# Kernel optimization log

Measured on AMD Instinct MI355X. Metric: run time of the kernel, lower is better.

Reference implementation:

```python
import jax, jax.numpy as jnp
import numpy as np

N_BRANCH, N_LAYER = 4, 3
B, T, D_IN = 4, 1024, 32
D_MODEL, D_INNER, D_STATE, D_CONV, DT_RANK = 128, 256, 16, 4, 8
EMBED = 64
MAX_NORM = 10.0  # safe_expmap0 tangent-norm clip
EPS = 1e-7


def setup_inputs() -> dict:
    key = jax.random.key(0)
    ks = jax.random.split(key, 12)
    def nrm(k, shp, s=0.02):
        return s * jax.random.normal(k, shp, dtype=jnp.float32)
    A_init = jnp.log(jnp.arange(1, D_STATE + 1, dtype=jnp.float32))
    return {
        "trend": jax.random.normal(ks[0], (B, T, D_IN), jnp.float32),
        "seasonal_coarse": jax.random.normal(ks[1], (B, T, D_IN), jnp.float32),
        "seasonal_fine": jax.random.normal(ks[2], (B, T, D_IN), jnp.float32),
        "residual": jax.random.normal(ks[3], (B, T, D_IN), jnp.float32),
        "W_ip": nrm(ks[4], (N_BRANCH, D_IN, D_MODEL)),
        "b_ip": jnp.zeros((N_BRANCH, D_MODEL), jnp.float32),
        "W_in": nrm(ks[5], (N_BRANCH, N_LAYER, D_MODEL, 2 * D_INNER)),
        "conv_w": nrm(ks[6], (N_BRANCH, N_LAYER, D_INNER, D_CONV), 0.1),
        "conv_b": jnp.zeros((N_BRANCH, N_LAYER, D_INNER), jnp.float32),
        "W_x": nrm(ks[7], (N_BRANCH, N_LAYER, D_INNER, DT_RANK + 2 * D_STATE)),
        "W_dt": nrm(ks[8], (N_BRANCH, N_LAYER, DT_RANK, D_INNER), 0.1),
        "b_dt": jnp.full((N_BRANCH, N_LAYER, D_INNER), -4.6, jnp.float32),  # softplus ~ 0.01
        "A_log": jnp.broadcast_to(A_init, (N_BRANCH, N_LAYER, D_INNER, D_STATE)),
        "D_param": jnp.ones((N_BRANCH, N_LAYER, D_INNER), jnp.float32),
        "W_out": nrm(ks[9], (N_BRANCH, N_LAYER, D_INNER, D_MODEL)),
        "W_op": nrm(ks[10], (N_BRANCH, D_MODEL, EMBED)),
        "b_op": jnp.zeros((N_BRANCH, EMBED), jnp.float32),
        "eff_scale": jnp.asarray(0.1, jnp.float32),
    }


def _mamba_layer(x, Win, cw, cb, Wx, Wdt, bdt, Alog, Dp, Wout):
    # x: [B, T, d_model]
    Tlen = x.shape[1]
    xz = x @ Win                                   # [B,T,2*di]
    xp, z = jnp.split(xz, 2, axis=-1)
    # causal depthwise conv1d, kernel D_CONV
    xpad = jnp.pad(xp, ((0, 0), (D_CONV - 1, 0), (0, 0)))
    xc = sum(xpad[:, k:k + Tlen, :] * cw[:, k] for k in range(D_CONV))
    xc = jax.nn.silu(xc + cb)                      # [B,T,di]
    dbl = xc @ Wx                                  # [B,T,r+2s]
    dt = jax.nn.softplus(dbl[..., :DT_RANK] @ Wdt + bdt)   # [B,T,di]
    Bm = dbl[..., DT_RANK:DT_RANK + D_STATE]       # [B,T,s]
    Cm = dbl[..., DT_RANK + D_STATE:]              # [B,T,s]
    A = -jnp.exp(Alog)                             # [di,s]
    dA = jnp.exp(dt[..., None] * A)                # [B,T,di,s]
    dBx = (dt * xc)[..., None] * Bm[:, :, None, :] # [B,T,di,s]

    def step(h, inp):
        dA_t, dBx_t, C_t = inp
        h = dA_t * h + dBx_t
        return h, jnp.einsum('bds,bs->bd', h, C_t)

    h0 = jnp.zeros((x.shape[0], D_INNER, D_STATE), x.dtype)
    _, ys = jax.lax.scan(step, h0, (jnp.swapaxes(dA, 0, 1),
                                     jnp.swapaxes(dBx, 0, 1),
                                     jnp.swapaxes(Cm, 0, 1)))
    y = jnp.swapaxes(ys, 0, 1) + Dp * xc
    return (y * jax.nn.silu(z)) @ Wout


def _embed(x, Wip, bip, Wins, cws, cbs, Wxs, Wdts, bdts, Alogs, Dps, Wouts, Wop, bop):
    h = x @ Wip + bip
    for l in range(N_LAYER):
        h = _mamba_layer(h, Wins[l], cws[l], cbs[l], Wxs[l], Wdts[l], bdts[l],
                         Alogs[l], Dps[l], Wouts[l])
    return h.mean(axis=1) @ Wop + bop              # [B, EMBED]


def _expmap0(v):
    # safe expmap0 on Lorentz (k=1): clip tangent norm at MAX_NORM
    n = jnp.linalg.norm(v, axis=-1, keepdims=True)
    nc = jnp.clip(n, EPS, MAX_NORM)
    v = v * (nc / jnp.maximum(n, EPS))
    return jnp.concatenate([jnp.cosh(nc), jnp.sinh(nc) / nc * v], axis=-1)


def _projx(x):
    sp = x[..., 1:]
    t = jnp.sqrt(1.0 + jnp.sum(sp * sp, axis=-1, keepdims=True))
    return jnp.concatenate([t, sp], axis=-1)


def _logmap0(x):
    sp = x[..., 1:]
    t = jnp.maximum(x[..., :1], 1.0 + EPS)
    d = jnp.arccosh(t)
    spn = jnp.maximum(jnp.linalg.norm(sp, axis=-1, keepdims=True), EPS)
    return d * sp / spn


def _forward(trend, seasonal_coarse, seasonal_fine, residual,
             W_ip, b_ip, W_in, conv_w, conv_b, W_x, W_dt, b_dt,
             A_log, D_param, W_out, W_op, b_op, eff_scale):
    xs = [trend, seasonal_coarse, seasonal_fine, residual]
    z_t = [
        _embed(xs[b], W_ip[b], b_ip[b], W_in[b], conv_w[b], conv_b[b], W_x[b],
               W_dt[b], b_dt[b], A_log[b], D_param[b], W_out[b], W_op[b], b_op[b])
        for b in range(N_BRANCH)
    ]
    es = jnp.tanh(eff_scale)
    z_h = [_projx(_expmap0(z * es)) for z in z_t]
    us = [_logmap0(zh) for zh in z_h]
    combined_tangent = us[0] + us[1] + us[2] + us[3]
    combined_h = _projx(_expmap0(combined_tangent * es))
    return (*z_t, *z_h, combined_tangent, combined_h)


def reference(trend, seasonal_coarse, seasonal_fine, residual,
              W_ip, b_ip, W_in, conv_w, conv_b, W_x, W_dt, b_dt,
              A_log, D_param, W_out, W_op, b_op, eff_scale):
    return _forward(trend, seasonal_coarse, seasonal_fine, residual,
                    W_ip, b_ip, W_in, conv_w, conv_b, W_x, W_dt, b_dt,
                    A_log, D_param, W_out, W_op, b_op, eff_scale)
```

## Files before the change

### kernel.cpp

```cpp
#include <hip/hip_runtime.h>
#include <math.h>

#define NBR 4
#define NLAY 3
#define Bk 4
#define Tk 1024
#define DIN 32
#define DMODEL 128
#define DINNER 256
#define DSTATE 16
#define DTRANK 8
#define EMBEDk 64
#define BT (Bk*Tk)
#define EPSF 1e-7f
#define MAXNF 10.0f
#define LCH 32
#define NCH (Tk/LCH)
#define UF 8
#define NWB 320

typedef __bf16 bf16x8 __attribute__((ext_vector_type(8)));
typedef float  f32x4  __attribute__((ext_vector_type(4)));
typedef unsigned short u16x8 __attribute__((ext_vector_type(8)));
typedef unsigned short u16x4 __attribute__((ext_vector_type(4)));

__device__ __forceinline__ float siluf(float x){ return x / (1.f + __expf(-x)); }
__device__ __forceinline__ float softplusf(float x){ return (x > 20.f) ? x : log1pf(__expf(x)); }
__device__ __forceinline__ unsigned short f2b(float x){
    union { float f; unsigned u; } v; v.f = x;
    unsigned r = v.u + 0x7FFF + ((v.u >> 16) & 1);
    return (unsigned short)(r >> 16);
}
__device__ __forceinline__ float b2f(unsigned short u){
    union { unsigned u; float f; } v; v.u = ((unsigned)u) << 16; return v.f;
}

__device__ __forceinline__ void dA_pow(float q, float* dA){
    dA[0] = q;             dA[1] = q * q;
    dA[2] = dA[1] * dA[0]; dA[3] = dA[1] * dA[1];
    dA[4] = dA[3] * dA[0]; dA[5] = dA[3] * dA[1];
    dA[6] = dA[3] * dA[2]; dA[7] = dA[3] * dA[3];
    #pragma unroll
    for (int s = 8; s < 16; ++s) dA[s] = dA[s - 8] * dA[7];
}
__device__ __forceinline__ void dA_exp(float dtv, const float* Aa, float* dA){
    #pragma unroll
    for (int s = 0; s < 16; ++s) dA[s] = __expf(dtv * Aa[s]);
}

template<int MODE>
__global__ __launch_bounds__(256) void bgemm_k(
    const unsigned short* __restrict__ Ab, long aBr, int K,
    const unsigned short* __restrict__ Bt, long bBr,
    float* __restrict__ C1, long c1Br,
    unsigned short* __restrict__ Cb, long cbBr,
    unsigned short* __restrict__ Cb2, long cb2Br,
    float* __restrict__ Mb,
    const float* __restrict__ bias, long biasBr)
{
    const int br = blockIdx.z;
    Ab += (long)br * aBr;
    Bt += (long)br * bBr;
    if (MODE == 0) { Cb += (long)br * cbBr; Cb2 += (long)br * cb2Br; }
    if (MODE == 3) { Cb += (long)br * cbBr; C1 += (long)br * c1Br;
                     bias += (long)br * biasBr; }
    if (MODE == 1) { Mb += (long)br * (Bk * DMODEL); }
    const int m0 = blockIdx.x * 64, n0 = blockIdx.y * 64;
    __shared__ __align__(16) unsigned short As[16 * 64 * 8];
    __shared__ __align__(16) unsigned short Bs[16 * 64 * 8];
    const int tid = threadIdx.x;
    const int lane = tid & 63, w = tid >> 6;
    const int wm = w >> 1, wn = w & 1;
    const int quad = lane >> 4, l15 = lane & 15;
    f32x4 acc00 = {0,0,0,0}, acc01 = {0,0,0,0}, acc10 = {0,0,0,0}, acc11 = {0,0,0,0};
    for (int kc = 0; kc < K; kc += 128) {
        #pragma unroll
        for (int it = 0; it < 4; ++it) {
            const int c = tid + it * 256;
            const int r = c & 63, kch = c >> 6;
            *(u16x8*)&As[(kch * 64 + r) * 8] =
                *(const u16x8*)(Ab + (long)(m0 + r) * K + kc + kch * 8);
            *(u16x8*)&Bs[(kch * 64 + r) * 8] =
                *(const u16x8*)(Bt + (long)(n0 + r) * K + kc + kch * 8);
        }
        __syncthreads();
        #pragma unroll
        for (int k0 = 0; k0 < 128; k0 += 32) {
            const int kch = (k0 >> 3) + quad;
            bf16x8 a0 = *(const bf16x8*)&As[(kch * 64 + wm * 32 +      l15) * 8];
            bf16x8 a1 = *(const bf16x8*)&As[(kch * 64 + wm * 32 + 16 + l15) * 8];
            bf16x8 b0 = *(const bf16x8*)&Bs[(kch * 64 + wn * 32 +      l15) * 8];
            bf16x8 b1 = *(const bf16x8*)&Bs[(kch * 64 + wn * 32 + 16 + l15) * 8];
            acc00 = __builtin_amdgcn_mfma_f32_16x16x32_bf16(a0, b0, acc00, 0, 0, 0);
            acc01 = __builtin_amdgcn_mfma_f32_16x16x32_bf16(a0, b1, acc01, 0, 0, 0);
            acc10 = __builtin_amdgcn_mfma_f32_16x16x32_bf16(a1, b0, acc10, 0, 0, 0);
            acc11 = __builtin_amdgcn_mfma_f32_16x16x32_bf16(a1, b1, acc11, 0, 0, 0);
        }
        __syncthreads();
    }
    if (MODE == 1) {
        float s0 = 0.f, s1 = 0.f;
        #pragma unroll
        for (int r = 0; r < 4; ++r) { s0 += acc00[r] + acc10[r];
                                      s1 += acc01[r] + acc11[r]; }
        const int bidx = m0 >> 10;
        atomicAdd(&Mb[bidx * DMODEL + n0 + wn * 32 + l15], s0);
        atomicAdd(&Mb[bidx * DMODEL + n0 + wn * 32 + 16 + l15], s1);
        return;
    }
    #pragma unroll
    for (int e = 0; e < 4; ++e) {
        f32x4 a = (e == 0) ? acc00 : (e == 1) ? acc01 : (e == 2) ? acc10 : acc11;
        const int msub = (e >> 1) * 16, nsub = (e & 1) * 16;
        const int col = n0 + wn * 32 + nsub + l15;
        #pragma unroll
        for (int r = 0; r < 4; ++r) {
            const int row = m0 + wm * 32 + msub + quad * 4 + r;
            const float v = a[r];
            if (MODE == 0) {
                if (n0 < 256) Cb[(long)row * 256 + col] = f2b(v);
                else          Cb2[(long)row * 256 + (col - 256)] = f2b(siluf(v));
            } else {
                if (col < 256)      Cb[(long)row * 256 + col] = f2b(softplusf(v + bias[col]));
                else if (col < 288) C1[(long)row * 32 + (col - 256)] = v;
            }
        }
    }
}

__device__ void transposeTile(const float* __restrict__ W,
                              unsigned short* __restrict__ o,
                              int Kd, int Nd, int n0, int k0, float* smem)
{
    float (*tile)[65] = (float(*)[65])smem;
    const int t = threadIdx.x;
    #pragma unroll
    for (int i = 0; i < 16; ++i) {
        int idx = t + i * 256;
        int kl = idx >> 6, nl = idx & 63;
        tile[kl][nl] = W[(long)(k0 + kl) * Nd + n0 + nl];
    }
    __syncthreads();
    #pragma unroll
    for (int i = 0; i < 16; ++i) {
        int idx = t + i * 256;
        int nl = idx >> 6, kl = idx & 63;
        o[(long)(n0 + nl) * Kd + k0 + kl] = f2b(tile[kl][nl]);
    }
}

__global__ __launch_bounds__(256) void prep_k(
    const float* __restrict__ W_in, const float* __restrict__ W_out,
    const float* __restrict__ W_x, const float* __restrict__ W_dt,
    const float* __restrict__ X0, const float* __restrict__ X1,
    const float* __restrict__ X2, const float* __restrict__ X3,
    const float* __restrict__ W_ip, const float* __restrict__ b_ip,
    unsigned short* __restrict__ Win0T, unsigned short* __restrict__ Wo2T,
    unsigned short* __restrict__ WcT, unsigned short* __restrict__ h_bf,
    unsigned short* __restrict__ WfT, unsigned* __restrict__ zbuf)
{
    __shared__ float smem[32 * 68 * 2];
    const int id = blockIdx.x;
    if (id < 64) {
        int br = id >> 4, rem = id & 15;
        int nt = rem & 7, kt = rem >> 3;
        transposeTile(W_in + (long)br * NLAY * DMODEL * 512,
                      Win0T + (long)br * 512 * DMODEL,
                      DMODEL, 512, nt * 64, kt * 64, smem);
    } else if (id < 96) {
        int id3 = id - 64;
        int br = id3 >> 3, rem = id3 & 7;
        int nt = rem & 1, kt = rem >> 1;
        transposeTile(W_out + ((long)br * NLAY + 2) * DINNER * DMODEL,
                      Wo2T + (long)br * DMODEL * DINNER,
                      DINNER, DMODEL, nt * 64, kt * 64, smem);
    } else if (id < 3936) {
        int id4 = id - 96;
        int bl = id4 / NWB, n = id4 % NWB;
        const int k = threadIdx.x;
        const float* WxP = W_x + (long)bl * DINNER * 40;
        float v;
        if (n < 256) {
            const float* WdtP = W_dt + (long)bl * DTRANK * DINNER;
            float s = 0.f;
            #pragma unroll
            for (int r = 0; r < 8; ++r)
                s = fmaf(WxP[k * 40 + r], WdtP[r * DINNER + n], s);
            v = s;
        } else if (n < 288) {
            v = WxP[k * 40 + 8 + (n - 256)];
        } else {
            v = 0.f;
        }
        WcT[(long)bl * NWB * DINNER + (long)n * DINNER + k] = f2b(v);
    } else if (id < 4448) {
        int id5 = id - 3936;
        int br = id5 >> 7, rem = id5 & 127;
        int m0 = (rem & 63) * 64, n0 = (rem >> 6) * 64;
        const float* A = (br == 1) ? X1 : (br == 2) ? X2 : (br == 3) ? X3 : X0;
        const float* Bw = W_ip + (long)br * DIN * DMODEL;
        const float* bias = b_ip + (long)br * DMODEL;
        unsigned short* Cb = h_bf + (long)br * BT * DMODEL;
        float (*As)[68] = (float(*)[68])smem;
        float (*Bs)[68] = (float(*)[68])(smem + 32 * 68);
        const int tid = threadIdx.x;
        const int tx = tid & 15, ty = tid >> 4;
        float acc[4][4] = {};
        #pragma unroll
        for (int it = 0; it < 2; ++it) {
            int idd = tid + it * 256;
            int r = idd >> 3, c4 = (idd & 7) << 2;
            float4 v = *(const float4*)(A + (long)(m0 + r) * DIN + c4);
            As[c4+0][r] = v.x; As[c4+1][r] = v.y; As[c4+2][r] = v.z; As[c4+3][r] = v.w;
            int rb = idd >> 4, cb = (idd & 15) << 2;
            *(float4*)&Bs[rb][cb] = *(const float4*)(Bw + (long)rb * DMODEL + n0 + cb);
        }
        __syncthreads();
        #pragma unroll
        for (int kk = 0; kk < 32; ++kk) {
            float4 a4 = *(const float4*)&As[kk][ty << 2];
            float4 b4 = *(const float4*)&Bs[kk][tx << 2];
            float av[4] = {a4.x, a4.y, a4.z, a4.w};
            float bv[4] = {b4.x, b4.y, b4.z, b4.w};
            #pragma unroll
            for (int i = 0; i < 4; ++i)
                #pragma unroll
                for (int j = 0; j < 4; ++j)
                    acc[i][j] = fmaf(av[i], bv[j], acc[i][j]);
        }
        const int col = n0 + (tx << 2);
        #pragma unroll
        for (int i = 0; i < 4; ++i) {
            const int row = m0 + (ty << 2) + i;
            #pragma unroll
            for (int j = 0; j < 4; ++j)
                Cb[(long)row * DMODEL + col + j] = f2b(acc[i][j] + bias[col + j]);
        }
    } else {
        if (id == 4448) {
            for (int i = threadIdx.x; i < 4096; i += 256) zbuf[i] = 0u;
        }
        int sid = id - 4448;
        int z = sid >> 5, rem = sid & 31;
        int mt = rem >> 3, nt = rem & 7;
        const int p = z >> 2, br = z & 3;
        const float* A  = W_out + (long)(br * NLAY + p) * DINNER * DMODEL;
        const float* Bw = W_in  + (long)(br * NLAY + p + 1) * DMODEL * 512;
        unsigned short* WfTz = WfT + (long)z * 512 * DINNER;
        const int m0 = mt * 64, n0 = nt * 64;
        float (*As)[68] = (float(*)[68])smem;
        float (*Bs)[68] = (float(*)[68])(smem + 32 * 68);
        const int tid = threadIdx.x;
        const int tx = tid & 15, ty = tid >> 4;
        float acc[4][4] = {};
        for (int kc = 0; kc < DMODEL; kc += 32) {
            #pragma unroll
            for (int it = 0; it < 2; ++it) {
                int idd = tid + it * 256;
                int r = idd >> 3, c4 = (idd & 7) << 2;
                float4 v = *(const float4*)(A + (long)(m0 + r) * DMODEL + kc + c4);
                As[c4+0][r] = v.x; As[c4+1][r] = v.y; As[c4+2][r] = v.z; As[c4+3][r] = v.w;
                int rb = idd >> 4, cb = (idd & 15) << 2;
                *(float4*)&Bs[rb][cb] = *(const float4*)(Bw + (long)(kc + rb) * 512 + n0 + cb);
            }
            __syncthreads();
            #pragma unroll
            for (int kk = 0; kk < 32; ++kk) {
                float4 a4 = *(const float4*)&As[kk][ty << 2];
                float4 b4 = *(const float4*)&Bs[kk][tx << 2];
                float av[4] = {a4.x, a4.y, a4.z, a4.w};
                float bv[4] = {b4.x, b4.y, b4.z, b4.w};
                #pragma unroll
                for (int i = 0; i < 4; ++i)
                    #pragma unroll
                    for (int j = 0; j < 4; ++j)
                        acc[i][j] = fmaf(av[i], bv[j], acc[i][j]);
            }
            __syncthreads();
        }
        const int row0 = m0 + (ty << 2);
        const int col0 = n0 + (tx << 2);
        #pragma unroll
        for (int j = 0; j < 4; ++j) {
            u16x4 t4;
            #pragma unroll
            for (int i = 0; i < 4; ++i) t4[i] = f2b(acc[i][j]);
            *(u16x4*)&WfTz[(long)(col0 + j) * DINNER + row0] = t4;
        }
    }
}

__global__ __launch_bounds__(256) void conv_k(
    const unsigned short* __restrict__ xp, const float* __restrict__ cw,
    const float* __restrict__ cb, unsigned short* __restrict__ xcb, int layer)
{
    const int br = blockIdx.y;
    const long base = (long)br * BT * DINNER;
    const int idx = blockIdx.x * 256 + threadIdx.x;
    const int d = idx & (DINNER - 1);
    const int row = idx >> 8;
    const int t = row & (Tk - 1);
    const float4 w4 = *(const float4*)(cw + ((long)(br * NLAY + layer) * DINNER + d) * 4);
    const float wv[4] = {w4.x, w4.y, w4.z, w4.w};
    float acc = cb[(br * NLAY + layer) * DINNER + d];
    const unsigned short* xpb = xp + base + idx;
    #pragma unroll
    for (int k = 0; k < 4; ++k) {
        int tt = t + k - 3;
        if (tt >= 0) acc = fmaf(b2f(xpb[(long)(k - 3) * DINNER]), wv[k], acc);
    }
    xcb[base + idx] = f2b(siluf(acc));
}

__global__ __launch_bounds__(256) void scan1_k(
    const unsigned short* __restrict__ dtb, const unsigned short* __restrict__ xcb,
    const float* __restrict__ bcb, const float* __restrict__ Alog,
    float* __restrict__ recbuf, int layer)
{
    const int c = blockIdx.x, b = blockIdx.y, br = blockIdx.z;
    const int d = threadIdx.x;
    const float* Ap = Alog + ((long)(br * NLAY + layer) * DINNER + d) * DSTATE;
    float Aa[16];
    bool pw = true;
    #pragma unroll
    for (int s = 0; s < 16; ++s) {
        Aa[s] = -__expf(Ap[s]);
        pw = pw && (fabsf(Aa[s] + (float)(s + 1)) < 1e-3f);
    }
    const long rbase = (long)br * BT + (long)b * Tk + (long)c * LCH;
    const unsigned short* dtp = dtb + rbase * DINNER + d;
    const unsigned short* xcp = xcb + rbase * DINNER + d;
    __shared__ float bcs[LCH * 32];
    {
        const float4* g = (const float4*)(bcb + rbase * 32);
        ((float4*)bcs)[d] = g[d];
    }
    float dtc[UF], xcc[UF];
    #pragma unroll
    for (int u = 0; u < UF; ++u) {
        dtc[u] = b2f(dtp[(long)u * DINNER]);
        xcc[u] = b2f(xcp[(long)u * DINNER]);
    }
    __syncthreads();
    float h[16];
    #pragma unroll
    for (int s = 0; s < 16; ++s) h[s] = 0.f;
    float sumdt = 0.f;
    for (int base = 0; base < LCH; base += UF) {
        const int nb = (base + UF < LCH) ? base + UF : base;
        float dtn[UF], xcn[UF];
        #pragma unroll
        for (int u = 0; u < UF; ++u) {
            dtn[u] = b2f(dtp[(long)(nb + u) * DINNER]);
            xcn[u] = b2f(xcp[(long)(nb + u) * DINNER]);
        }
        #pragma unroll
        for (int u = 0; u < UF; ++u) {
            const int t = base + u;
            const float dtv = dtc[u];
            const float dtxc = dtv * xcc[u];
            sumdt += dtv;
            float dA[16];
            if (pw) dA_pow(__expf(-dtv), dA);
            else    dA_exp(dtv, Aa, dA);
            const float* bcT = bcs + t * 32;
            #pragma unroll
            for (int s = 0; s < 16; ++s)
                h[s] = fmaf(dA[s], h[s], dtxc * bcT[s]);
        }
        #pragma unroll
        for (int u = 0; u < UF; ++u) { dtc[u] = dtn[u]; xcc[u] = xcn[u]; }
    }
    float* sb = recbuf + (((long)(br * 4 + b) * (NCH - 1) + c) * 17) * 256 + d;
    #pragma unroll
    for (int s = 0; s < 16; ++s) sb[s * 256] = h[s];
    sb[16 * 256] = sumdt;
}

__global__ __launch_bounds__(256) void scan3_k(
    const unsigned short* __restrict__ dtb, const unsigned short* __restrict__ xcb,
    const float* __restrict__ bcb, const unsigned short* __restrict__ zb,
    const float* __restrict__ Alog, const float* __restrict__ Dpar,
    const float* __restrict__ recbuf, unsigned short* __restrict__ yzb, int layer)
{
    const int c = blockIdx.x, b = blockIdx.y, br = blockIdx.z;
    const int d = threadIdx.x;
    const float* Ap = Alog + ((long)(br * NLAY + layer) * DINNER + d) * DSTATE;
    float Aa[16];
    bool pw = true;
    #pragma unroll
    for (int s = 0; s < 16; ++s) {
        Aa[s] = -__expf(Ap[s]);
        pw = pw && (fabsf(Aa[s] + (float)(s + 1)) < 1e-3f);
    }
    float h[16];
    #pragma unroll
    for (int s = 0; s < 16; ++s) h[s] = 0.f;
    if (c > 0) {
        const float* recB = recbuf + ((long)(br * 4 + b) * (NCH - 1)) * 17 * 256 + d;
        float rh[16], rs;
        #pragma unroll
        for (int s = 0; s < 16; ++s) rh[s] = recB[s * 256];
        rs = recB[16 * 256];
        for (int cc = 0; cc < c; ++cc) {
            float nh[16], ns = 0.f;
            if (cc + 1 < c) {
                const float* r2 = recB + (long)(cc + 1) * 17 * 256;
                #pragma unroll
                for (int s = 0; s < 16; ++s) nh[s] = r2[s * 256];
                ns = r2[16 * 256];
            } else {
                #pragma unroll
                for (int s = 0; s < 16; ++s) nh[s] = 0.f;
            }
            float P[16];
            if (pw) dA_pow(__expf(-rs), P);
            else    dA_exp(rs, Aa, P);
            #pragma unroll
            for (int s = 0; s < 16; ++s) h[s] = fmaf(h[s], P[s], rh[s]);
            #pragma unroll
            for (int s = 0; s < 16; ++s) rh[s] = nh[s];
            rs = ns;
        }
    }
    const float Dp = Dpar[(br * NLAY + layer) * DINNER + d];
    const long rbase = (long)br * BT + (long)b * Tk + (long)c * LCH;
    const unsigned short* dtp = dtb + rbase * DINNER + d;
    const unsigned short* xcp = xcb + rbase * DINNER + d;
    const unsigned short* zp  = zb  + rbase * DINNER + d;
    unsigned short* yp = yzb + rbase * DINNER + d;
    __shared__ float bcs[LCH * 32];
    {
        const float4* g = (const float4*)(bcb + rbase * 32);
        ((float4*)bcs)[d] = g[d];
    }
    float dtc[UF], xcc[UF], zc[UF];
    #pragma unroll
    for (int u = 0; u < UF; ++u) {
        dtc[u] = b2f(dtp[(long)u * DINNER]);
        xcc[u] = b2f(xcp[(long)u * DINNER]);
        zc[u]  = b2f(zp[(long)u * DINNER]);
    }
    __syncthreads();
    for (int base = 0; base < LCH; base += UF) {
        const int nb = (base + UF < LCH) ? base + UF : base;
        float dtn[UF], xcn[UF], zn[UF];
        #pragma unroll
        for (int u = 0; u < UF; ++u) {
            dtn[u] = b2f(dtp[(long)(nb + u) * DINNER]);
            xcn[u] = b2f(xcp[(long)(nb + u) * DINNER]);
            zn[u]  = b2f(zp[(long)(nb + u) * DINNER]);
        }
        #pragma unroll
        for (int u = 0; u < UF; ++u) {
            const int t = base + u;
            const float dtv = dtc[u], xcv = xcc[u];
            const float dtxc = dtv * xcv;
            float dA[16];
            if (pw) dA_pow(__expf(-dtv), dA);
            else    dA_exp(dtv, Aa, dA);
            const float* bcT = bcs + t * 32;
            #pragma unroll
            for (int s = 0; s < 16; ++s)
                h[s] = fmaf(dA[s], h[s], dtxc * bcT[s]);
            float y0 = 0.f, y1 = 0.f, y2 = 0.f, y3 = 0.f;
            #pragma unroll
            for (int s = 0; s < 16; s += 4) {
                y0 = fmaf(h[s+0], bcT[16+s+0], y0);
                y1 = fmaf(h[s+1], bcT[16+s+1], y1);
                y2 = fmaf(h[s+2], bcT[16+s+2], y2);
                y3 = fmaf(h[s+3], bcT[16+s+3], y3);
            }
            const float y = (y0 + y1) + (y2 + y3) + Dp * xcv;
            yp[(long)t * DINNER] = f2b(y * zc[u]);
        }
        #pragma unroll
        for (int u = 0; u < UF; ++u) { dtc[u] = dtn[u]; xcc[u] = xcn[u]; zc[u] = zn[u]; }
    }
}

__global__ __launch_bounds__(64) void final_k(
    const float* __restrict__ Mb, const float* __restrict__ Wop,
    const float* __restrict__ bop, float* __restrict__ out,
    const float* __restrict__ eff)
{
    __shared__ float hm[NBR * Bk * DMODEL];
    __shared__ float zts[NBR * Bk * EMBEDk];
    __shared__ float us[NBR][Bk][EMBEDk];
    const int t = threadIdx.x;
    for (int i = t; i < NBR * Bk * DMODEL; i += 64) hm[i] = Mb[i] * (1.0f / Tk);
    __syncthreads();
    for (int br = 0; br < NBR; ++br) {
        const float* wp = Wop + (long)br * DMODEL * EMBEDk + t;
        const float bb = bop[br * EMBEDk + t];
        for (int b = 0; b < Bk; ++b) {
            const float* hmp = &hm[(br * Bk + b) * DMODEL];
            float acc = bb;
            for (int k = 0; k < DMODEL; ++k) acc = fmaf(hmp[k], wp[k * EMBEDk], acc);
            out[(br * Bk + b) * EMBEDk + t] = acc;
            zts[(br * Bk + b) * EMBEDk + t] = acc;
        }
    }
    __syncthreads();
    const float es = tanhf(eff[0]);
    if (t < 16) {
        const int br = t >> 2, b = t & 3;
        const float* z = &zts[(br * Bk + b) * EMBEDk];
        float n2 = 0.f;
        for (int e = 0; e < EMBEDk; ++e) { float v = z[e] * es; n2 = fmaf(v, v, n2); }
        const float n  = sqrtf(n2);
        const float nc = fminf(fmaxf(n, EPSF), MAXNF);
        const float sc = nc / fmaxf(n, EPSF);
        const float sh = sinhf(nc) / nc;
        const float fac = es * sc * sh;
        float* zh = out + 1024 + br * (Bk * (EMBEDk + 1)) + b * (EMBEDk + 1);
        float sp2 = 0.f;
        for (int e = 0; e < EMBEDk; ++e) {
            float spv = z[e] * fac;
            sp2 = fmaf(spv, spv, sp2);
            zh[1 + e] = spv;
            us[br][b][e] = spv;
        }
        const float t0 = sqrtf(1.f + sp2);
        zh[0] = t0;
        const float dd  = acoshf(fmaxf(t0, 1.f + EPSF));
        const float spn = fmaxf(sqrtf(sp2), EPSF);
        const float rr  = dd / spn;
        for (int e = 0; e < EMBEDk; ++e) us[br][b][e] *= rr;
    }
    __syncthreads();
    if (t < 4) {
        const int b = t;
        float ct[EMBEDk];
        float* cto = out + 2064 + b * EMBEDk;
        for (int e = 0; e < EMBEDk; ++e) {
            float v = us[0][b][e] + us[1][b][e] + us[2][b][e] + us[3][b][e];
            ct[e] = v; cto[e] = v;
        }
        float n2 = 0.f;
        for (int e = 0; e < EMBEDk; ++e) { float v = ct[e] * es; n2 = fmaf(v, v, n2); }
        const float n  = sqrtf(n2);
        const float nc = fminf(fmaxf(n, EPSF), MAXNF);
        const float sc = nc / fmaxf(n, EPSF);
        const float sh = sinhf(nc) / nc;
        const float fac = es * sc * sh;
        float* ch = out + 2320 + b * (EMBEDk + 1);
        float sp2 = 0.f;
        for (int e = 0; e < EMBEDk; ++e) {
            float spv = ct[e] * fac;
            sp2 = fmaf(spv, spv, sp2);
            ch[1 + e] = spv;
        }
        ch[0] = sqrtf(1.f + sp2);
    }
}

extern "C" void kernel_launch(void* const* d_in, const int* in_sizes, int n_in,
                              void* d_out, int out_size, void* d_ws, size_t ws_size,
                              hipStream_t stream)
{
    const float* X0 = (const float*)d_in[0];
    const float* X1 = (const float*)d_in[1];
    const float* X2 = (const float*)d_in[2];
    const float* X3 = (const float*)d_in[3];
    const float* W_ip   = (const float*)d_in[4];
    const float* b_ip   = (const float*)d_in[5];
    const float* W_in   = (const float*)d_in[6];
    const float* conv_w = (const float*)d_in[7];
    const float* conv_b = (const float*)d_in[8];
    const float* W_x    = (const float*)d_in[9];
    const float* W_dt   = (const float*)d_in[10];
    const float* b_dt   = (const float*)d_in[11];
    const float* A_log  = (const float*)d_in[12];
    const float* D_par  = (const float*)d_in[13];
    const float* W_out  = (const float*)d_in[14];
    const float* W_op   = (const float*)d_in[15];
    const float* b_op   = (const float*)d_in[16];
    const float* eff    = (const float*)d_in[17];
    float* out = (float*)d_out;
    float* ws  = (float*)d_ws;

    float* meanb  = ws + 1024;
    float* buf_bc = ws + 4096;
    float* recbuf = buf_bc + (long)NBR * BT * 32;
    unsigned short* dt_bf = (unsigned short*)(recbuf + (long)16 * (NCH - 1) * 17 * 256);
    unsigned short* h_bf  = dt_bf + (long)NBR * BT * DINNER;
    unsigned short* xp_bf = h_bf  + (long)NBR * BT * DMODEL;
    unsigned short* z_bf  = xp_bf + (long)NBR * BT * DINNER;
    unsigned short* xc_bf = z_bf  + (long)NBR * BT * DINNER;
    unsigned short* yz_bf = xc_bf + (long)NBR * BT * DINNER;
    unsigned short* Win0T = yz_bf + (long)NBR * BT * DINNER;
    unsigned short* WfT   = Win0T + (long)NBR * 512 * DMODEL;
    unsigned short* Wo2T  = WfT   + (long)8 * 512 * DINNER;
    unsigned short* WcT   = Wo2T  + (long)NBR * DMODEL * DINNER;

    prep_k<<<4704, 256, 0, stream>>>(
        W_in, W_out, W_x, W_dt, X0, X1, X2, X3, W_ip, b_ip,
        Win0T, Wo2T, WcT, h_bf, WfT, (unsigned*)ws);

    for (int l = 0; l < NLAY; ++l) {
        if (l == 0) {
            bgemm_k<0><<<dim3(BT / 64, 8, NBR), 256, 0, stream>>>(
                h_bf, (long)BT * DMODEL, DMODEL, Win0T, (long)512 * DMODEL,
                nullptr, 0,
                xp_bf, (long)BT * DINNER, z_bf, (long)BT * DINNER,
                nullptr, nullptr, 0);
        } else {
            bgemm_k<0><<<dim3(BT / 64, 8, NBR), 256, 0, stream>>>(
                yz_bf, (long)BT * DINNER, DINNER,
                WfT + (long)(l - 1) * 4 * 512 * DINNER, (long)512 * DINNER,
                nullptr, 0,
                xp_bf, (long)BT * DINNER, z_bf, (long)BT * DINNER,
                nullptr, nullptr, 0);
        }
        conv_k<<<dim3((BT * DINNER) / 256, NBR), 256, 0, stream>>>(
            xp_bf, conv_w, conv_b, xc_bf, l);
        bgemm_k<3><<<dim3(BT / 64, NWB / 64, NBR), 256, 0, stream>>>(
            xc_bf, (long)BT * DINNER, DINNER,
            WcT + (long)l * NWB * DINNER, (long)NLAY * NWB * DINNER,
            buf_bc, (long)BT * 32,
            dt_bf, (long)BT * DINNER, nullptr, 0,
            nullptr, b_dt + l * DINNER, (long)NLAY * DINNER);
        scan1_k<<<dim3(NCH - 1, Bk, NBR), 256, 0, stream>>>(
            dt_bf, xc_bf, buf_bc, A_log, recbuf, l);
        scan3_k<<<dim3(NCH, Bk, NBR), 256, 0, stream>>>(
            dt_bf, xc_bf, buf_bc, z_bf, A_log, D_par, recbuf, yz_bf, l);
        if (l == NLAY - 1) {
            bgemm_k<1><<<dim3(BT / 64, DMODEL / 64, NBR), 256, 0, stream>>>(
                yz_bf, (long)BT * DINNER, DINNER,
                Wo2T, (long)DMODEL * DINNER,
                nullptr, 0, nullptr, 0, nullptr, 0,
                meanb, nullptr, 0);
        }
    }

    final_k<<<1, 64, 0, stream>>>(meanb, W_op, b_op, out, eff);
}
```

Baseline: 482.0 us.

## Fuse causal conv into dt/BC GEMM and scans; fold final out-projection into mean

Removes the standalone conv kernel and xc buffer: the depthwise causal conv plus SiLU is recomputed on the fly inside the dt/BC GEMM's A-tile load and inside both scan kernels from xp. The last layer's out-projection GEMM is replaced by accumulating the time-sum of yz per channel in the scan via atomics, then applying W_out to the mean in the final kernel, using linearity. This cuts memory traffic and two launches, at the cost of redundant conv arithmetic, larger register arrays in the scans, and a heavier single-block final kernel.

```diff
diff --git a/kernel.cpp b/kernel.cpp
--- a/kernel.cpp
+++ b/kernel.cpp
@@ -16,7 +16,6 @@
 #define MAXNF 10.0f
 #define LCH 32
 #define NCH (Tk/LCH)
-#define UF 8
 #define NWB 320
 
 typedef __bf16 bf16x8 __attribute__((ext_vector_type(8)));
@@ -48,23 +47,16 @@
     for (int s = 0; s < 16; ++s) dA[s] = __expf(dtv * Aa[s]);
 }
 
-template<int MODE>
-__global__ __launch_bounds__(256) void bgemm_k(
+__global__ __launch_bounds__(256) void xz_k(
     const unsigned short* __restrict__ Ab, long aBr, int K,
     const unsigned short* __restrict__ Bt, long bBr,
-    float* __restrict__ C1, long c1Br,
-    unsigned short* __restrict__ Cb, long cbBr,
-    unsigned short* __restrict__ Cb2, long cb2Br,
-    float* __restrict__ Mb,
-    const float* __restrict__ bias, long biasBr)
+    unsigned short* __restrict__ Cxp, unsigned short* __restrict__ Cz)
 {
     const int br = blockIdx.z;
     Ab += (long)br * aBr;
     Bt += (long)br * bBr;
-    if (MODE == 0) { Cb += (long)br * cbBr; Cb2 += (long)br * cb2Br; }
-    if (MODE == 3) { Cb += (long)br * cbBr; C1 += (long)br * c1Br;
-                     bias += (long)br * biasBr; }
-    if (MODE == 1) { Mb += (long)br * (Bk * DMODEL); }
+    Cxp += (long)br * BT * DINNER;
+    Cz  += (long)br * BT * DINNER;
     const int m0 = blockIdx.x * 64, n0 = blockIdx.y * 64;
     __shared__ __align__(16) unsigned short As[16 * 64 * 8];
     __shared__ __align__(16) unsigned short Bs[16 * 64 * 8];
@@ -98,16 +90,6 @@
         }
         __syncthreads();
     }
-    if (MODE == 1) {
-        float s0 = 0.f, s1 = 0.f;
-        #pragma unroll
-        for (int r = 0; r < 4; ++r) { s0 += acc00[r] + acc10[r];
-                                      s1 += acc01[r] + acc11[r]; }
-        const int bidx = m0 >> 10;
-        atomicAdd(&Mb[bidx * DMODEL + n0 + wn * 32 + l15], s0);
-        atomicAdd(&Mb[bidx * DMODEL + n0 + wn * 32 + 16 + l15], s1);
-        return;
-    }
     #pragma unroll
     for (int e = 0; e < 4; ++e) {
         f32x4 a = (e == 0) ? acc00 : (e == 1) ? acc01 : (e == 2) ? acc10 : acc11;
@@ -117,13 +99,97 @@
         for (int r = 0; r < 4; ++r) {
             const int row = m0 + wm * 32 + msub + quad * 4 + r;
             const float v = a[r];
-            if (MODE == 0) {
-                if (n0 < 256) Cb[(long)row * 256 + col] = f2b(v);
-                else          Cb2[(long)row * 256 + (col - 256)] = f2b(siluf(v));
-            } else {
-                if (col < 256)      Cb[(long)row * 256 + col] = f2b(softplusf(v + bias[col]));
-                else if (col < 288) C1[(long)row * 32 + (col - 256)] = v;
+            if (n0 < 256) Cxp[(long)row * 256 + col] = f2b(v);
+            else          Cz[(long)row * 256 + (col - 256)] = f2b(siluf(v));
+        }
+    }
+}
+
+__global__ __launch_bounds__(256) void dtbc_k(
+    const unsigned short* __restrict__ xp, const unsigned short* __restrict__ WcT,
+    const float* __restrict__ conv_w, const float* __restrict__ conv_b,
+    const float* __restrict__ b_dt,
+    unsigned short* __restrict__ dtb, float* __restrict__ bcb, int layer)
+{
+    const int br = blockIdx.z;
+    const int bl = br * NLAY + layer;
+    xp  += (long)br * BT * DINNER;
+    WcT += (long)bl * NWB * DINNER;
+    dtb += (long)br * BT * DINNER;
+    bcb += (long)br * BT * 32;
+    const float* bias = b_dt + (long)bl * DINNER;
+    const int m0 = blockIdx.x * 64, n0 = blockIdx.y * 64;
+    __shared__ __align__(16) unsigned short As[16 * 64 * 8];
+    __shared__ __align__(16) unsigned short Bs[16 * 64 * 8];
+    __shared__ float cw_s[256][4];
+    __shared__ float cb_s[256];
+    const int tid = threadIdx.x;
+    {
+        const float4 w = *(const float4*)(conv_w + ((long)bl * DINNER + tid) * 4);
+        cw_s[tid][0] = w.x; cw_s[tid][1] = w.y; cw_s[tid][2] = w.z; cw_s[tid][3] = w.w;
+        cb_s[tid] = conv_b[bl * DINNER + tid];
+    }
+    __syncthreads();
+    const int lane = tid & 63, w = tid >> 6;
+    const int wm = w >> 1, wn = w & 1;
+    const int quad = lane >> 4, l15 = lane & 15;
+    f32x4 acc00 = {0,0,0,0}, acc01 = {0,0,0,0}, acc10 = {0,0,0,0}, acc11 = {0,0,0,0};
+    for (int kc = 0; kc < DINNER; kc += 128) {
+        #pragma unroll
+        for (int it = 0; it < 4; ++it) {
+            const int c = tid + it * 256;
+            const int r = c & 63, kch = c >> 6;
+            const int row = m0 + r;
+            const int tb = row & (Tk - 1);
+            const int d0 = kc + kch * 8;
+            u16x8 xr[4];
+            #pragma unroll
+            for (int k = 0; k < 4; ++k) {
+                if (tb + k - 3 >= 0)
+                    xr[k] = *(const u16x8*)(xp + (long)(row + k - 3) * DINNER + d0);
+                else
+                    xr[k] = (u16x8){0,0,0,0,0,0,0,0};
             }
+            u16x8 o;
+            #pragma unroll
+            for (int j = 0; j < 8; ++j) {
+                const int d = d0 + j;
+                float a = cb_s[d];
+                #pragma unroll
+                for (int k = 0; k < 4; ++k)
+                    a = fmaf(b2f(xr[k][j]), cw_s[d][k], a);
+                o[j] = f2b(siluf(a));
+            }
+            *(u16x8*)&As[(kch * 64 + r) * 8] = o;
+            *(u16x8*)&Bs[(kch * 64 + r) * 8] =
+                *(const u16x8*)(WcT + (long)(n0 + r) * DINNER + kc + kch * 8);
+        }
+        __syncthreads();
+        #pragma unroll
+        for (int k0 = 0; k0 < 128; k0 += 32) {
+            const int kch = (k0 >> 3) + quad;
+            bf16x8 a0 = *(const bf16x8*)&As[(kch * 64 + wm * 32 +      l15) * 8];
+            bf16x8 a1 = *(const bf16x8*)&As[(kch * 64 + wm * 32 + 16 + l15) * 8];
+            bf16x8 b0 = *(const bf16x8*)&Bs[(kch * 64 + wn * 32 +      l15) * 8];
+            bf16x8 b1 = *(const bf16x8*)&Bs[(kch * 64 + wn * 32 + 16 + l15) * 8];
+            acc00 = __builtin_amdgcn_mfma_f32_16x16x32_bf16(a0, b0, acc00, 0, 0, 0);
+            acc01 = __builtin_amdgcn_mfma_f32_16x16x32_bf16(a0, b1, acc01, 0, 0, 0);
+            acc10 = __builtin_amdgcn_mfma_f32_16x16x32_bf16(a1, b0, acc10, 0, 0, 0);
+            acc11 = __builtin_amdgcn_mfma_f32_16x16x32_bf16(a1, b1, acc11, 0, 0, 0);
+        }
+        __syncthreads();
+    }
+    #pragma unroll
+    for (int e = 0; e < 4; ++e) {
+        f32x4 a = (e == 0) ? acc00 : (e == 1) ? acc01 : (e == 2) ? acc10 : acc11;
+        const int msub = (e >> 1) * 16, nsub = (e & 1) * 16;
+        const int col = n0 + wn * 32 + nsub + l15;
+        #pragma unroll
+        for (int r = 0; r < 4; ++r) {
+            const int row = m0 + wm * 32 + msub + quad * 4 + r;
+            const float v = a[r];
+            if (col < 256)      dtb[(long)row * 256 + col] = f2b(softplusf(v + bias[col]));
+            else if (col < 288) bcb[(long)row * 32 + (col - 256)] = v;
         }
     }
 }
@@ -155,9 +221,9 @@
     const float* __restrict__ X0, const float* __restrict__ X1,
     const float* __restrict__ X2, const float* __restrict__ X3,
     const float* __restrict__ W_ip, const float* __restrict__ b_ip,
-    unsigned short* __restrict__ Win0T, unsigned short* __restrict__ Wo2T,
-    unsigned short* __restrict__ WcT, unsigned short* __restrict__ h_bf,
-    unsigned short* __restrict__ WfT, unsigned* __restrict__ zbuf)
+    unsigned short* __restrict__ Win0T, unsigned short* __restrict__ WcT,
+    unsigned short* __restrict__ h_bf, unsigned short* __restrict__ WfT,
+    unsigned* __restrict__ zbuf)
 {
     __shared__ float smem[32 * 68 * 2];
     const int id = blockIdx.x;
@@ -167,15 +233,8 @@
         transposeTile(W_in + (long)br * NLAY * DMODEL * 512,
                       Win0T + (long)br * 512 * DMODEL,
                       DMODEL, 512, nt * 64, kt * 64, smem);
-    } else if (id < 96) {
-        int id3 = id - 64;
-        int br = id3 >> 3, rem = id3 & 7;
-        int nt = rem & 1, kt = rem >> 1;
-        transposeTile(W_out + ((long)br * NLAY + 2) * DINNER * DMODEL,
-                      Wo2T + (long)br * DMODEL * DINNER,
-                      DINNER, DMODEL, nt * 64, kt * 64, smem);
-    } else if (id < 3936) {
-        int id4 = id - 96;
+    } else if (id < 3904) {
+        int id4 = id - 64;
         int bl = id4 / NWB, n = id4 % NWB;
         const int k = threadIdx.x;
         const float* WxP = W_x + (long)bl * DINNER * 40;
@@ -193,8 +252,8 @@
             v = 0.f;
         }
         WcT[(long)bl * NWB * DINNER + (long)n * DINNER + k] = f2b(v);
-    } else if (id < 4448) {
-        int id5 = id - 3936;
+    } else if (id < 4416) {
+        int id5 = id - 3904;
         int br = id5 >> 7, rem = id5 & 127;
         int m0 = (rem & 63) * 64, n0 = (rem >> 6) * 64;
         const float* A = (br == 1) ? X1 : (br == 2) ? X2 : (br == 3) ? X3 : X0;
@@ -237,10 +296,10 @@
                 Cb[(long)row * DMODEL + col + j] = f2b(acc[i][j] + bias[col + j]);
         }
     } else {
-        if (id == 4448) {
+        if (id == 4416) {
             for (int i = threadIdx.x; i < 4096; i += 256) zbuf[i] = 0u;
         }
-        int sid = id - 4448;
+        int sid = id - 4416;
         int z = sid >> 5, rem = sid & 31;
         int mt = rem >> 3, nt = rem & 7;
         const int p = z >> 2, br = z & 3;
@@ -290,36 +349,16 @@
     }
 }
 
-__global__ __launch_bounds__(256) void conv_k(
-    const unsigned short* __restrict__ xp, const float* __restrict__ cw,
-    const float* __restrict__ cb, unsigned short* __restrict__ xcb, int layer)
-{
-    const int br = blockIdx.y;
-    const long base = (long)br * BT * DINNER;
-    const int idx = blockIdx.x * 256 + threadIdx.x;
-    const int d = idx & (DINNER - 1);
-    const int row = idx >> 8;
-    const int t = row & (Tk - 1);
-    const float4 w4 = *(const float4*)(cw + ((long)(br * NLAY + layer) * DINNER + d) * 4);
-    const float wv[4] = {w4.x, w4.y, w4.z, w4.w};
-    float acc = cb[(br * NLAY + layer) * DINNER + d];
-    const unsigned short* xpb = xp + base + idx;
-    #pragma unroll
-    for (int k = 0; k < 4; ++k) {
-        int tt = t + k - 3;
-        if (tt >= 0) acc = fmaf(b2f(xpb[(long)(k - 3) * DINNER]), wv[k], acc);
-    }
-    xcb[base + idx] = f2b(siluf(acc));
-}
-
 __global__ __launch_bounds__(256) void scan1_k(
-    const unsigned short* __restrict__ dtb, const unsigned short* __restrict__ xcb,
-    const float* __restrict__ bcb, const float* __restrict__ Alog,
+    const unsigned short* __restrict__ dtb, const unsigned short* __restrict__ xpb,
+    const float* __restrict__ bcb, const float* __restrict__ cw,
+    const float* __restrict__ cbp, const float* __restrict__ Alog,
     float* __restrict__ recbuf, int layer)
 {
     const int c = blockIdx.x, b = blockIdx.y, br = blockIdx.z;
     const int d = threadIdx.x;
-    const float* Ap = Alog + ((long)(br * NLAY + layer) * DINNER + d) * DSTATE;
+    const int bl = br * NLAY + layer;
+    const float* Ap = Alog + ((long)bl * DINNER + d) * DSTATE;
     float Aa[16];
     bool pw = true;
     #pragma unroll
@@ -328,48 +367,48 @@
         pw = pw && (fabsf(Aa[s] + (float)(s + 1)) < 1e-3f);
     }
     const long rbase = (long)br * BT + (long)b * Tk + (long)c * LCH;
+    __shared__ float bcs[LCH * 32];
+    ((float4*)bcs)[d] = ((const float4*)(bcb + rbase * 32))[d];
+    const unsigned short* xpp = xpb + rbase * DINNER + d;
     const unsigned short* dtp = dtb + rbase * DINNER + d;
-    const unsigned short* xcp = xcb + rbase * DINNER + d;
-    __shared__ float bcs[LCH * 32];
-    {
-        const float4* g = (const float4*)(bcb + rbase * 32);
-        ((float4*)bcs)[d] = g[d];
-    }
-    float dtc[UF], xcc[UF];
-    #pragma unroll
-    for (int u = 0; u < UF; ++u) {
-        dtc[u] = b2f(dtp[(long)u * DINNER]);
-        xcc[u] = b2f(xcp[(long)u * DINNER]);
+    const float4 w4 = *(const float4*)(cw + ((long)bl * DINNER + d) * 4);
+    const float cbv = cbp[bl * DINNER + d];
+    float xpv[LCH + 3];
+    #pragma unroll
+    for (int i = 0; i < LCH + 3; ++i) {
+        const int tl = i - 3;
+        xpv[i] = (c * LCH + tl >= 0) ? b2f(xpp[(long)tl * DINNER]) : 0.f;
+    }
+    float dtv[LCH];
+    #pragma unroll
+    for (int t = 0; t < LCH; ++t) dtv[t] = b2f(dtp[(long)t * DINNER]);
+    float xcv[LCH];
+    #pragma unroll
+    for (int t = 0; t < LCH; ++t) {
+        float a = cbv;
+        a = fmaf(xpv[t],     w4.x, a);
+        a = fmaf(xpv[t + 1], w4.y, a);
+        a = fmaf(xpv[t + 2], w4.z, a);
+        a = fmaf(xpv[t + 3], w4.w, a);
+        xcv[t] = siluf(a);
     }
     __syncthreads();
     float h[16];
     #pragma unroll
     for (int s = 0; s < 16; ++s) h[s] = 0.f;
     float sumdt = 0.f;
-    for (int base = 0; base < LCH; base += UF) {
-        const int nb = (base + UF < LCH) ? base + UF : base;
-        float dtn[UF], xcn[UF];
-        #pragma unroll
-        for (int u = 0; u < UF; ++u) {
-            dtn[u] = b2f(dtp[(long)(nb + u) * DINNER]);
-            xcn[u] = b2f(xcp[(long)(nb + u) * DINNER]);
-        }
-        #pragma unroll
-        for (int u = 0; u < UF; ++u) {
-            const int t = base + u;
-            const float dtv = dtc[u];
-            const float dtxc = dtv * xcc[u];
-            sumdt += dtv;
-            float dA[16];
-            if (pw) dA_pow(__expf(-dtv), dA);
-            else    dA_exp(dtv, Aa, dA);
-            const float* bcT = bcs + t * 32;
-            #pragma unroll
-            for (int s = 0; s < 16; ++s)
-                h[s] = fmaf(dA[s], h[s], dtxc * bcT[s]);
-        }
-        #pragma unroll
-        for (int u = 0; u < UF; ++u) { dtc[u] = dtn[u]; xcc[u] = xcn[u]; }
+    #pragma unroll
+    for (int t = 0; t < LCH; ++t) {
+        const float dtval = dtv[t];
+        const float dtxc = dtval * xcv[t];
+        sumdt += dtval;
+        float dA[16];
+        if (pw) dA_pow(__expf(-dtval), dA);
+        else    dA_exp(dtval, Aa, dA);
+        const float* bcT = bcs + t * 32;
+        #pragma unroll
+        for (int s = 0; s < 16; ++s)
+            h[s] = fmaf(dA[s], h[s], dtxc * bcT[s]);
     }
     float* sb = recbuf + (((long)(br * 4 + b) * (NCH - 1) + c) * 17) * 256 + d;
     #pragma unroll
@@ -378,14 +417,17 @@
 }
 
 __global__ __launch_bounds__(256) void scan3_k(
-    const unsigned short* __restrict__ dtb, const unsigned short* __restrict__ xcb,
+    const unsigned short* __restrict__ dtb, const unsigned short* __restrict__ xpb,
     const float* __restrict__ bcb, const unsigned short* __restrict__ zb,
+    const float* __restrict__ cw, const float* __restrict__ cbp,
     const float* __restrict__ Alog, const float* __restrict__ Dpar,
-    const float* __restrict__ recbuf, unsigned short* __restrict__ yzb, int layer)
+    const float* __restrict__ recbuf, unsigned short* __restrict__ yzb,
+    float* __restrict__ Macc, int layer)
 {
     const int c = blockIdx.x, b = blockIdx.y, br = blockIdx.z;
     const int d = threadIdx.x;
-    const float* Ap = Alog + ((long)(br * NLAY + layer) * DINNER + d) * DSTATE;
+    const int bl = br * NLAY + layer;
+    const float* Ap = Alog + ((long)bl * DINNER + d) * DSTATE;
     float Aa[16];
     bool pw = true;
     #pragma unroll
@@ -393,6 +435,38 @@
         Aa[s] = -__expf(Ap[s]);
         pw = pw && (fabsf(Aa[s] + (float)(s + 1)) < 1e-3f);
     }
+    const long rbase = (long)br * BT + (long)b * Tk + (long)c * LCH;
+    __shared__ float bcs[LCH * 32];
+    ((float4*)bcs)[d] = ((const float4*)(bcb + rbase * 32))[d];
+    const unsigned short* xpp = xpb + rbase * DINNER + d;
+    const unsigned short* dtp = dtb + rbase * DINNER + d;
+    const unsigned short* zp  = zb  + rbase * DINNER + d;
+    unsigned short* yp = yzb + rbase * DINNER + d;
+    const float4 w4 = *(const float4*)(cw + ((long)bl * DINNER + d) * 4);
+    const float cbv = cbp[bl * DINNER + d];
+    float xpv[LCH + 3];
+    #pragma unroll
+    for (int i = 0; i < LCH + 3; ++i) {
+        const int tl = i - 3;
+        xpv[i] = (c * LCH + tl >= 0) ? b2f(xpp[(long)tl * DINNER]) : 0.f;
+    }
+    float dtv[LCH], zv[LCH];
+    #pragma unroll
+    for (int t = 0; t < LCH; ++t) {
+        dtv[t] = b2f(dtp[(long)t * DINNER]);
+        zv[t]  = b2f(zp[(long)t * DINNER]);
+    }
+    float xcv[LCH];
+    #pragma unroll
+    for (int t = 0; t < LCH; ++t) {
+        float a = cbv;
+        a = fmaf(xpv[t],     w4.x, a);
+        a = fmaf(xpv[t + 1], w4.y, a);
+        a = fmaf(xpv[t + 2], w4.z, a);
+        a = fmaf(xpv[t + 3], w4.w, a);
+        xcv[t] = siluf(a);
+    }
+    __syncthreads();
     float h[16];
     #pragma unroll
     for (int s = 0; s < 16; ++s) h[s] = 0.f;
@@ -423,83 +497,66 @@
             rs = ns;
         }
     }
-    const float Dp = Dpar[(br * NLAY + layer) * DINNER + d];
-    const long rbase = (long)br * BT + (long)b * Tk + (long)c * LCH;
-    const unsigned short* dtp = dtb + rbase * DINNER + d;
-    const unsigned short* xcp = xcb + rbase * DINNER + d;
-    const unsigned short* zp  = zb  + rbase * DINNER + d;
-    unsigned short* yp = yzb + rbase * DINNER + d;
-    __shared__ float bcs[LCH * 32];
-    {
-        const float4* g = (const float4*)(bcb + rbase * 32);
-        ((float4*)bcs)[d] = g[d];
-    }
-    float dtc[UF], xcc[UF], zc[UF];
-    #pragma unroll
-    for (int u = 0; u < UF; ++u) {
-        dtc[u] = b2f(dtp[(long)u * DINNER]);
-        xcc[u] = b2f(xcp[(long)u * DINNER]);
-        zc[u]  = b2f(zp[(long)u * DINNER]);
-    }
-    __syncthreads();
-    for (int base = 0; base < LCH; base += UF) {
-        const int nb = (base + UF < LCH) ? base + UF : base;
-        float dtn[UF], xcn[UF], zn[UF];
-        #pragma unroll
-        for (int u = 0; u < UF; ++u) {
-            dtn[u] = b2f(dtp[(long)(nb + u) * DINNER]);
-            xcn[u] = b2f(xcp[(long)(nb + u) * DINNER]);
-            zn[u]  = b2f(zp[(long)(nb + u) * DINNER]);
-        }
-        #pragma unroll
-        for (int u = 0; u < UF; ++u) {
-            const int t = base + u;
-            const float dtv = dtc[u], xcv = xcc[u];
-            const float dtxc = dtv * xcv;
-            float dA[16];
-            if (pw) dA_pow(__expf(-dtv), dA);
-            else    dA_exp(dtv, Aa, dA);
-            const float* bcT = bcs + t * 32;
-            #pragma unroll
-            for (int s = 0; s < 16; ++s)
-                h[s] = fmaf(dA[s], h[s], dtxc * bcT[s]);
-            float y0 = 0.f, y1 = 0.f, y2 = 0.f, y3 = 0.f;
-            #pragma unroll
-            for (int s = 0; s < 16; s += 4) {
-                y0 = fmaf(h[s+0], bcT[16+s+0], y0);
-                y1 = fmaf(h[s+1], bcT[16+s+1], y1);
-                y2 = fmaf(h[s+2], bcT[16+s+2], y2);
-                y3 = fmaf(h[s+3], bcT[16+s+3], y3);
-            }
-            const float y = (y0 + y1) + (y2 + y3) + Dp * xcv;
-            yp[(long)t * DINNER] = f2b(y * zc[u]);
-        }
-        #pragma unroll
-        for (int u = 0; u < UF; ++u) { dtc[u] = dtn[u]; xcc[u] = xcn[u]; zc[u] = zn[u]; }
-    }
-}
-
-__global__ __launch_bounds__(64) void final_k(
-    const float* __restrict__ Mb, const float* __restrict__ Wop,
-    const float* __restrict__ bop, float* __restrict__ out,
-    const float* __restrict__ eff)
-{
-    __shared__ float hm[NBR * Bk * DMODEL];
-    __shared__ float zts[NBR * Bk * EMBEDk];
+    const float Dp = Dpar[bl * DINNER + d];
+    float yzsum = 0.f;
+    #pragma unroll
+    for (int t = 0; t < LCH; ++t) {
+        const float dtval = dtv[t], xcval = xcv[t];
+        const float dtxc = dtval * xcval;
+        float dA[16];
+        if (pw) dA_pow(__expf(-dtval), dA);
+        else    dA_exp(dtval, Aa, dA);
+        const float* bcT = bcs + t * 32;
+        #pragma unroll
+        for (int s = 0; s < 16; ++s)
+            h[s] = fmaf(dA[s], h[s], dtxc * bcT[s]);
+        float y0 = 0.f, y1 = 0.f, y2 = 0.f, y3 = 0.f;
+        #pragma unroll
+        for (int s = 0; s < 16; s += 4) {
+            y0 = fmaf(h[s+0], bcT[16+s+0], y0);
+            y1 = fmaf(h[s+1], bcT[16+s+1], y1);
+            y2 = fmaf(h[s+2], bcT[16+s+2], y2);
+            y3 = fmaf(h[s+3], bcT[16+s+3], y3);
+        }
+        const float y = (y0 + y1) + (y2 + y3) + Dp * xcval;
+        const float yz = y * zv[t];
+        yzsum += yz;
+        yp[(long)t * DINNER] = f2b(yz);
+    }
+    if (Macc) atomicAdd(&Macc[(br * 4 + b) * DINNER + d], yzsum);
+}
+
+__global__ __launch_bounds__(256) void final_k(
+    const float* __restrict__ Macc, const float* __restrict__ W_out,
+    const float* __restrict__ Wop, const float* __restrict__ bop,
+    float* __restrict__ out, const float* __restrict__ eff)
+{
+    __shared__ float ms[16 * 256];
+    __shared__ float mh[16 * 128];
+    __shared__ float zts[16 * 64];
     __shared__ float us[NBR][Bk][EMBEDk];
     const int t = threadIdx.x;
-    for (int i = t; i < NBR * Bk * DMODEL; i += 64) hm[i] = Mb[i] * (1.0f / Tk);
-    __syncthreads();
-    for (int br = 0; br < NBR; ++br) {
-        const float* wp = Wop + (long)br * DMODEL * EMBEDk + t;
-        const float bb = bop[br * EMBEDk + t];
-        for (int b = 0; b < Bk; ++b) {
-            const float* hmp = &hm[(br * Bk + b) * DMODEL];
-            float acc = bb;
-            for (int k = 0; k < DMODEL; ++k) acc = fmaf(hmp[k], wp[k * EMBEDk], acc);
-            out[(br * Bk + b) * EMBEDk + t] = acc;
-            zts[(br * Bk + b) * EMBEDk + t] = acc;
-        }
+    for (int i = t; i < 16 * 256; i += 256) ms[i] = Macc[i] * (1.0f / Tk);
+    __syncthreads();
+    for (int o = t; o < 16 * 128; o += 256) {
+        const int seq = o >> 7, dm = o & 127;
+        const int br = seq >> 2;
+        const float* W2 = W_out + (long)(br * NLAY + 2) * DINNER * DMODEL;
+        float a = 0.f;
+        for (int dd = 0; dd < DINNER; ++dd)
+            a = fmaf(ms[seq * 256 + dd], W2[dd * DMODEL + dm], a);
+        mh[o] = a;
+    }
+    __syncthreads();
+    for (int o = t; o < 16 * 64; o += 256) {
+        const int seq = o >> 6, e = o & 63;
+        const int br = seq >> 2;
+        float a = bop[br * EMBEDk + e];
+        const float* wp = Wop + (long)br * DMODEL * EMBEDk;
+        for (int k = 0; k < DMODEL; ++k)
+            a = fmaf(mh[seq * 128 + k], wp[k * EMBEDk + e], a);
+        out[o] = a;
+        zts[o] = a;
     }
     __syncthreads();
     const float es = tanhf(eff[0]);
@@ -580,59 +637,41 @@
     float* out = (float*)d_out;
     float* ws  = (float*)d_ws;
 
-    float* meanb  = ws + 1024;
+    float* Macc   = ws;
     float* buf_bc = ws + 4096;
     float* recbuf = buf_bc + (long)NBR * BT * 32;
     unsigned short* dt_bf = (unsigned short*)(recbuf + (long)16 * (NCH - 1) * 17 * 256);
     unsigned short* h_bf  = dt_bf + (long)NBR * BT * DINNER;
     unsigned short* xp_bf = h_bf  + (long)NBR * BT * DMODEL;
     unsigned short* z_bf  = xp_bf + (long)NBR * BT * DINNER;
-    unsigned short* xc_bf = z_bf  + (long)NBR * BT * DINNER;
-    unsigned short* yz_bf = xc_bf + (long)NBR * BT * DINNER;
+    unsigned short* yz_bf = z_bf  + (long)NBR * BT * DINNER;
     unsigned short* Win0T = yz_bf + (long)NBR * BT * DINNER;
     unsigned short* WfT   = Win0T + (long)NBR * 512 * DMODEL;
-    unsigned short* Wo2T  = WfT   + (long)8 * 512 * DINNER;
-    unsigned short* WcT   = Wo2T  + (long)NBR * DMODEL * DINNER;
-
-    prep_k<<<4704, 256, 0, stream>>>(
+    unsigned short* WcT   = WfT   + (long)8 * 512 * DINNER;
+
+    prep_k<<<4672, 256, 0, stream>>>(
         W_in, W_out, W_x, W_dt, X0, X1, X2, X3, W_ip, b_ip,
-        Win0T, Wo2T, WcT, h_bf, WfT, (unsigned*)ws);
+        Win0T, WcT, h_bf, WfT, (unsigned*)ws);
 
     for (int l = 0; l < NLAY; ++l) {
         if (l == 0) {
-            bgemm_k<0><<<dim3(BT / 64, 8, NBR), 256, 0, stream>>>(
-                h_bf, (long)BT * DMODEL, DMODEL, Win0T, (long)512 * DMODEL,
-                nullptr, 0,
-                xp_bf, (long)BT * DINNER, z_bf, (long)BT * DINNER,
-                nullptr, nullptr, 0);
+            xz_k<<<dim3(BT / 64, 8, NBR), 256, 0, stream>>>(
+                h_bf, (long)BT * DMODEL, DMODEL,
+                Win0T, (long)512 * DMODEL, xp_bf, z_bf);
         } else {
-            bgemm_k<0><<<dim3(BT / 64, 8, NBR), 256, 0, stream>>>(
+            xz_k<<<dim3(BT / 64, 8, NBR), 256, 0, stream>>>(
                 yz_bf, (long)BT * DINNER, DINNER,
                 WfT + (long)(l - 1) * 4 * 512 * DINNER, (long)512 * DINNER,
-                nullptr, 0,
-                xp_bf, (long)BT * DINNER, z_bf, (long)BT * DINNER,
-                nullptr, nullptr, 0);
-        }
-        conv_k<<<dim3((BT * DINNER) / 256, NBR), 256, 0, stream>>>(
-            xp_bf, conv_w, conv_b, xc_bf, l);
-        bgemm_k<3><<<dim3(BT / 64, NWB / 64, NBR), 256, 0, stream>>>(
-            xc_bf, (long)BT * DINNER, DINNER,
-            WcT + (long)l * NWB * DINNER, (long)NLAY * NWB * DINNER,
-            buf_bc, (long)BT * 32,
-            dt_bf, (long)BT * DINNER, nullptr, 0,
-            nullptr, b_dt + l * DINNER, (long)NLAY * DINNER);
+                xp_bf, z_bf);
+        }
+        dtbc_k<<<dim3(BT / 64, NWB / 64, NBR), 256, 0, stream>>>(
+            xp_bf, WcT, conv_w, conv_b, b_dt, dt_bf, buf_bc, l);
         scan1_k<<<dim3(NCH - 1, Bk, NBR), 256, 0, stream>>>(
-            dt_bf, xc_bf, buf_bc, A_log, recbuf, l);
+            dt_bf, xp_bf, buf_bc, conv_w, conv_b, A_log, recbuf, l);
         scan3_k<<<dim3(NCH, Bk, NBR), 256, 0, stream>>>(
-            dt_bf, xc_bf, buf_bc, z_bf, A_log, D_par, recbuf, yz_bf, l);
-        if (l == NLAY - 1) {
-            bgemm_k<1><<<dim3(BT / 64, DMODEL / 64, NBR), 256, 0, stream>>>(
-                yz_bf, (long)BT * DINNER, DINNER,
-                Wo2T, (long)DMODEL * DINNER,
-                nullptr, 0, nullptr, 0, nullptr, 0,
-                meanb, nullptr, 0);
-        }
-    }
-
-    final_k<<<1, 64, 0, stream>>>(meanb, W_op, b_op, out, eff);
-}
+            dt_bf, xp_bf, buf_bc, z_bf, conv_w, conv_b, A_log, D_par,
+            recbuf, yz_bf, (l == NLAY - 1) ? Macc : nullptr, l);
+    }
+
+    final_k<<<1, 256, 0, stream>>>(Macc, W_out, W_op, b_op, out, eff);
+}
```

Measured after the change: 1.066 ms. +121.2%, slower.
